# Optimization experiments

Measured on AMD Instinct MI355X. Metric: run time of the kernel, lower is better.

## Reference

```python
import jax, jax.numpy as jnp
import numpy as np

MAX_WORDS = 2048  # max word tokens per sequence (static num_segments)


def setup_inputs() -> dict:
    key = jax.random.key(0)
    k1, k2, k3, k4 = jax.random.split(key, 4)
    B, S, H, D = 8, 4096, 768, 1024
    embeddings = jax.random.normal(k1, (B, S, H), dtype=jnp.float32)
    proj_w = jax.random.normal(k2, (H, D), dtype=jnp.float32) * 0.02
    proj_b = jax.random.normal(k3, (D,), dtype=jnp.float32) * 0.02
    masks = jnp.ones((B, S), dtype=jnp.int32)
    word_ids = jnp.sort(jax.random.randint(k4, (B, S), 0, MAX_WORDS), axis=-1)
    return {"embeddings": embeddings, "proj_w": proj_w, "proj_b": proj_b,
            "masks": masks, "word_ids": word_ids}


def reference(embeddings, proj_w, proj_b, masks, word_ids):
    B, S, H = embeddings.shape
    W = MAX_WORDS
    # Flatten batch+word into one segment id space: seg in [0, B*W)
    seg = (word_ids + jnp.arange(B, dtype=word_ids.dtype)[:, None] * W).reshape(-1)
    flat_emb = embeddings.reshape(B * S, H)
    # segment-sum of embeddings over subwords of each word  -> (B, W, H)
    sum_emb = jax.ops.segment_sum(flat_emb, seg, num_segments=B * W).reshape(B, W, H)
    ones = jnp.ones((B * S,), dtype=jnp.float32)
    counts = jax.ops.segment_sum(ones, seg, num_segments=B * W).reshape(B, W)
    mcounts = jax.ops.segment_sum(masks.reshape(-1).astype(jnp.float32), seg,
                                  num_segments=B * W).reshape(B, W)
    # word is valid iff it has >=1 subword and ALL its subwords have mask==1
    valid = (counts > 0) & (counts == mcounts)
    mean_emb = sum_emb / jnp.maximum(counts, 1.0)[..., None]
    token_embeddings = jnp.where(valid[..., None], mean_emb, 0.0)  # (B, W, H)
    token_masks = valid.astype(jnp.int32)                          # (B, W)
    # projection: hidden 768 -> config.hidden_size 1024
    out = jnp.einsum('bwh,hd->bwd', token_embeddings, proj_w) + proj_b
    return out, token_masks
```

## Files before the change

### kernel.cpp

```cpp
#include <hip/hip_runtime.h>
#include <hip/hip_bf16.h>
#include <stdint.h>

#define Bn 8
#define Sn 4096
#define Hn 768
#define Dn 1024
#define Wn 2048

typedef __attribute__((ext_vector_type(8))) short short8;
typedef __attribute__((ext_vector_type(4))) short short4v;
typedef __attribute__((ext_vector_type(4))) float floatx4;

__device__ __forceinline__ void load_lds16(const void* g, void* l) {
  __builtin_amdgcn_global_load_lds(
      (const __attribute__((address_space(1))) void*)g,
      (__attribute__((address_space(3))) void*)l, 16, 0, 0);
}

__device__ __forceinline__ int lb4096(const int* __restrict__ a, int x, int lane) {
  const int p = a[lane << 6];
  const unsigned long long m1 = __ballot(p < x);
  const int n1 = __popcll(m1);
  const int base = (n1 > 0 ? n1 - 1 : 0) << 6;
  const int q = a[base + lane];
  const unsigned long long m2 = __ballot(q < x);
  return base + __popcll(m2);
}

__global__ __launch_bounds__(256) void k_front(const float* __restrict__ emb,
                                               const float* __restrict__ pw,
                                               const int* __restrict__ masks,
                                               const int* __restrict__ wid,
                                               __hip_bfloat16* __restrict__ wb,
                                               __hip_bfloat16* __restrict__ wa,
                                               float* __restrict__ out_masks) {
  const int bid = blockIdx.x;
  if (bid >= 4096) {
    __shared__ float tile[32][33];
    const int bt = bid - 4096;
    const int d0 = (bt % 32) * 32, h0 = (bt / 32) * 32;
    const int tx = threadIdx.x & 31, ty = threadIdx.x >> 5;
#pragma unroll
    for (int i = 0; i < 32; i += 8)
      tile[ty + i][tx] = pw[(size_t)(h0 + ty + i) * Dn + d0 + tx];
    __syncthreads();
#pragma unroll
    for (int i = 0; i < 32; i += 8)
      wb[(size_t)(d0 + ty + i) * Hn + h0 + tx] = (__hip_bfloat16)tile[tx][ty + i];
    return;
  }

  const int b = bid >> 9;
  const int wave = threadIdx.x >> 6, lane = threadIdx.x & 63;
  const int w = (bid & 511) * 4 + wave;

  const int* wbi = wid + (size_t)b * Sn;
  const int start = lb4096(wbi, w, lane);
  const int end = lb4096(wbi, w + 1, lane);
  const int count = end - start;

  const int* mb = masks + (size_t)b * Sn;
  bool allone = true;
  for (int s0 = start; s0 < end; s0 += 64) {
    const int idx = s0 + lane;
    allone = allone && ((idx < end) ? (mb[idx] == 1) : true);
  }
  const bool valid = (count > 0) && __all(allone);
  const float inv = valid ? 1.0f / (float)count : 0.0f;

  floatx4 sum[3] = {{0.f, 0.f, 0.f, 0.f}, {0.f, 0.f, 0.f, 0.f}, {0.f, 0.f, 0.f, 0.f}};
  const float* eb = emb + (size_t)b * Sn * Hn;
  int s = start;
  for (; s + 1 < end; s += 2) {
    const floatx4* r0 = (const floatx4*)(eb + (size_t)s * Hn);
    const floatx4* r1 = (const floatx4*)(eb + (size_t)(s + 1) * Hn);
#pragma unroll
    for (int j = 0; j < 3; ++j) sum[j] += r0[j * 64 + lane];
#pragma unroll
    for (int j = 0; j < 3; ++j) sum[j] += r1[j * 64 + lane];
  }
  if (s < end) {
    const floatx4* r0 = (const floatx4*)(eb + (size_t)s * Hn);
#pragma unroll
    for (int j = 0; j < 3; ++j) sum[j] += r0[j * 64 + lane];
  }

  const size_t rowbase = ((size_t)b * Wn + w) * Hn;
#pragma unroll
  for (int j = 0; j < 3; ++j) {
    short4v o;
#pragma unroll
    for (int c = 0; c < 4; ++c) {
      __hip_bfloat16 h = (__hip_bfloat16)(sum[j][c] * inv);
      o[c] = *reinterpret_cast<short*>(&h);
    }
    *(short4v*)&wa[rowbase + (size_t)(j * 64 + lane) * 4] = o;
  }
  if (lane == 0) out_masks[(size_t)b * Wn + w] = valid ? 1.0f : 0.0f;
}

__global__ __launch_bounds__(256) void k_gemm(const short* __restrict__ A,
                                              const short* __restrict__ Bt,
                                              const float* __restrict__ bias,
                                              float* __restrict__ out) {
  constexpr int K = Hn;
  constexpr int N = Dn;
  __shared__ __align__(16) short lsA[2][128 * 32];
  __shared__ __align__(16) short lsB[2][128 * 32];

  const int t = threadIdx.x;
  const int lane = t & 63, wave = t >> 6;
  const int wm = wave >> 1, wn = wave & 1;
  const int lane16 = lane & 15, quad = lane >> 4;

  const int linear = blockIdx.x;
  const int xcd = linear & 7;
  const int o = linear >> 3;
  const int m0 = (xcd * 16 + (o >> 3)) * 128;
  const int n0 = (o & 7) * 128;

  const int lrow = t >> 2;
  const int lcol = (t & 3) * 8;
  const short* gA0 = A + (size_t)(m0 + lrow) * K + lcol;
  const short* gB0 = Bt + (size_t)(n0 + lrow) * K + lcol;
  const int loff = lrow * 32 + lcol;

  float bv[4];
#pragma unroll
  for (int ni = 0; ni < 4; ++ni)
    bv[ni] = bias[n0 + wn * 64 + ni * 16 + lane16];

  floatx4 acc[4][4];
#pragma unroll
  for (int i = 0; i < 4; ++i)
#pragma unroll
    for (int j = 0; j < 4; ++j) acc[i][j] = (floatx4){0.f, 0.f, 0.f, 0.f};

  for (int k0 = 0; k0 < K; k0 += 64) {
    load_lds16(gA0 + k0,                    &lsA[0][loff]);
    load_lds16(gA0 + (size_t)64 * K + k0,   &lsA[0][loff + 64 * 32]);
    load_lds16(gA0 + k0 + 32,               &lsA[1][loff]);
    load_lds16(gA0 + (size_t)64 * K + k0 + 32, &lsA[1][loff + 64 * 32]);
    load_lds16(gB0 + k0,                    &lsB[0][loff]);
    load_lds16(gB0 + (size_t)64 * K + k0,   &lsB[0][loff + 64 * 32]);
    load_lds16(gB0 + k0 + 32,               &lsB[1][loff]);
    load_lds16(gB0 + (size_t)64 * K + k0 + 32, &lsB[1][loff + 64 * 32]);
    __syncthreads();

#pragma unroll
    for (int sp = 0; sp < 2; ++sp) {
      short8 af[4], bf[4];
#pragma unroll
      for (int mi = 0; mi < 4; ++mi)
        af[mi] = *(const short8*)&lsA[sp][(wm * 64 + mi * 16 + lane16) * 32 + quad * 8];
#pragma unroll
      for (int ni = 0; ni < 4; ++ni)
        bf[ni] = *(const short8*)&lsB[sp][(wn * 64 + ni * 16 + lane16) * 32 + quad * 8];

#pragma unroll
      for (int mi = 0; mi < 4; ++mi)
#pragma unroll
        for (int ni = 0; ni < 4; ++ni)
          acc[mi][ni] = __builtin_amdgcn_mfma_f32_16x16x32_bf16(af[mi], bf[ni], acc[mi][ni], 0, 0, 0);
    }
    __syncthreads();
  }

#pragma unroll
  for (int mi = 0; mi < 4; ++mi) {
#pragma unroll
    for (int ni = 0; ni < 4; ++ni) {
      const int n = n0 + wn * 64 + ni * 16 + lane16;
#pragma unroll
      for (int r = 0; r < 4; ++r) {
        const int m = m0 + wm * 64 + mi * 16 + quad * 4 + r;
        __builtin_nontemporal_store(acc[mi][ni][r] + bv[ni], &out[(size_t)m * N + n]);
      }
    }
  }
}

extern "C" void kernel_launch(void* const* d_in, const int* in_sizes, int n_in,
                              void* d_out, int out_size, void* d_ws, size_t ws_size,
                              hipStream_t stream) {
  const float* emb    = (const float*)d_in[0];
  const float* proj_w = (const float*)d_in[1];
  const float* proj_b = (const float*)d_in[2];
  const int*   masks  = (const int*)d_in[3];
  const int*   wid    = (const int*)d_in[4];

  float* out = (float*)d_out;
  float* out_masks = out + (size_t)Bn * Wn * Dn;

  __hip_bfloat16* wb = (__hip_bfloat16*)d_ws;
  __hip_bfloat16* wa = wb + (size_t)Dn * Hn;

  k_front<<<dim3(4096 + 768), 256, 0, stream>>>(emb, proj_w, masks, wid, wb, wa,
                                                out_masks);

  k_gemm<<<dim3(1024), 256, 0, stream>>>((const short*)wa, (const short*)wb,
                                         proj_b, out);
}
```

Baseline: 211.7 us.

## Rewrite GEMM with 256x256 tiles, swizzled LDS, and overlapped prefetch

Replaces the 128x128 GEMM tile with a 256x256 tile per 512-thread block, using 128 KB of dynamic LDS double-buffered across K steps of 64. LDS rows are XOR-swizzled to avoid bank conflicts. The next tile's global-to-LDS loads are issued between MFMA phases, and s_setprio raises priority during the MFMA sections. The aim is more data reuse and latency hiding, at the cost of only 256 blocks (one wave of work on 256 CUs) and higher register pressure.

Measured after the change: 205.0 us. 1.03x faster.

```diff
diff --git a/kernel.cpp b/kernel.cpp
--- a/kernel.cpp
+++ b/kernel.cpp
@@ -100,82 +100,122 @@
   if (lane == 0) out_masks[(size_t)b * Wn + w] = valid ? 1.0f : 0.0f;
 }
 
-__global__ __launch_bounds__(256) void k_gemm(const short* __restrict__ A,
-                                              const short* __restrict__ Bt,
-                                              const float* __restrict__ bias,
-                                              float* __restrict__ out) {
-  constexpr int K = Hn;
-  constexpr int N = Dn;
-  __shared__ __align__(16) short lsA[2][128 * 32];
-  __shared__ __align__(16) short lsB[2][128 * 32];
+constexpr int GK = Hn;
+constexpr int TS = 256 * 64;
+constexpr int kGemmLds = 2 * 2 * TS * (int)sizeof(short);
+static_assert(kGemmLds == 131072, "LDS budget");
+
+__global__ __launch_bounds__(512, 2) void k_gemm(const short* __restrict__ A,
+                                                 const short* __restrict__ Bt,
+                                                 const float* __restrict__ bias,
+                                                 float* __restrict__ out) {
+  extern __shared__ __align__(16) short ls[];
 
   const int t = threadIdx.x;
   const int lane = t & 63, wave = t >> 6;
-  const int wm = wave >> 1, wn = wave & 1;
+  const int wm = wave >> 2, wn = wave & 3;
   const int lane16 = lane & 15, quad = lane >> 4;
-
-  const int linear = blockIdx.x;
-  const int xcd = linear & 7;
-  const int o = linear >> 3;
-  const int m0 = (xcd * 16 + (o >> 3)) * 128;
-  const int n0 = (o & 7) * 128;
-
-  const int lrow = t >> 2;
-  const int lcol = (t & 3) * 8;
-  const short* gA0 = A + (size_t)(m0 + lrow) * K + lcol;
-  const short* gB0 = Bt + (size_t)(n0 + lrow) * K + lcol;
-  const int loff = lrow * 32 + lcol;
+  const int swz = lane16 & 7;
+
+  const int mt = blockIdx.x & 63, nt = blockIdx.x >> 6;
+  const int m0 = mt * 256, n0 = nt * 256;
+
+  const int rS = t >> 3;
+  const int csw = ((t & 7) ^ (rS & 7)) * 8;
+  const short* gAs = A + (size_t)(m0 + rS) * GK + csw;
+  const short* gBs = Bt + (size_t)(n0 + rS) * GK + csw;
+  const int dst0 = t * 8;
+
+  auto stage_a = [&](int buf, int kt) {
+    short* d = ls + buf * 2 * TS + dst0;
+    const short* g = gAs + kt * 64;
+#pragma unroll
+    for (int j = 0; j < 4; ++j) load_lds16(g + (size_t)(j * 64) * GK, d + j * 4096);
+  };
+  auto stage_b = [&](int buf, int kt) {
+    short* d = ls + buf * 2 * TS + TS + dst0;
+    const short* g = gBs + kt * 64;
+#pragma unroll
+    for (int j = 0; j < 4; ++j) load_lds16(g + (size_t)(j * 64) * GK, d + j * 4096);
+  };
+
+  auto ld_a = [&](short8(&af)[4][2], int qm, const short* bufA) {
+#pragma unroll
+    for (int mf = 0; mf < 4; ++mf)
+#pragma unroll
+      for (int ks = 0; ks < 2; ++ks)
+        af[mf][ks] = *(const short8*)&bufA[(wm * 128 + qm * 64 + mf * 16 + lane16) * 64 +
+                                           ((((ks << 2) | quad) ^ swz) << 3)];
+  };
+  auto ld_b = [&](short8(&bf)[2][2], int qn, const short* bufB) {
+#pragma unroll
+    for (int nf = 0; nf < 2; ++nf)
+#pragma unroll
+      for (int ks = 0; ks < 2; ++ks)
+        bf[nf][ks] = *(const short8*)&bufB[(wn * 64 + qn * 32 + nf * 16 + lane16) * 64 +
+                                           ((((ks << 2) | quad) ^ swz) << 3)];
+  };
+
+  floatx4 acc[8][4];
+#pragma unroll
+  for (int i = 0; i < 8; ++i)
+#pragma unroll
+    for (int j = 0; j < 4; ++j) acc[i][j] = (floatx4){0.f, 0.f, 0.f, 0.f};
+
+  auto mm = [&](short8(&af)[4][2], short8(&bf)[2][2], int qm, int qn) {
+    __builtin_amdgcn_s_setprio(1);
+#pragma unroll
+    for (int mf = 0; mf < 4; ++mf)
+#pragma unroll
+      for (int nf = 0; nf < 2; ++nf)
+#pragma unroll
+        for (int ks = 0; ks < 2; ++ks)
+          acc[qm * 4 + mf][qn * 2 + nf] = __builtin_amdgcn_mfma_f32_16x16x32_bf16(
+              af[mf][ks], bf[nf][ks], acc[qm * 4 + mf][qn * 2 + nf], 0, 0, 0);
+    __builtin_amdgcn_s_setprio(0);
+  };
+
+  stage_a(0, 0);
+  stage_b(0, 0);
+  __syncthreads();
+
+#pragma unroll 1
+  for (int kt = 0; kt < 12; ++kt) {
+    const short* bufA = ls + (kt & 1) * 2 * TS;
+    const short* bufB = bufA + TS;
+    const int nb = (kt + 1) & 1;
+    short8 af[4][2], b0[2][2], b1[2][2];
+
+    ld_a(af, 0, bufA);
+    ld_b(b0, 0, bufB);
+    if (kt < 11) stage_a(nb, kt + 1);
+    mm(af, b0, 0, 0);
+
+    ld_b(b1, 1, bufB);
+    if (kt < 11) stage_b(nb, kt + 1);
+    mm(af, b1, 0, 1);
+
+    ld_a(af, 1, bufA);
+    mm(af, b1, 1, 1);
+
+    mm(af, b0, 1, 0);
+
+    __syncthreads();
+  }
 
   float bv[4];
 #pragma unroll
-  for (int ni = 0; ni < 4; ++ni)
-    bv[ni] = bias[n0 + wn * 64 + ni * 16 + lane16];
-
-  floatx4 acc[4][4];
-#pragma unroll
-  for (int i = 0; i < 4; ++i)
-#pragma unroll
-    for (int j = 0; j < 4; ++j) acc[i][j] = (floatx4){0.f, 0.f, 0.f, 0.f};
-
-  for (int k0 = 0; k0 < K; k0 += 64) {
-    load_lds16(gA0 + k0,                    &lsA[0][loff]);
-    load_lds16(gA0 + (size_t)64 * K + k0,   &lsA[0][loff + 64 * 32]);
-    load_lds16(gA0 + k0 + 32,               &lsA[1][loff]);
-    load_lds16(gA0 + (size_t)64 * K + k0 + 32, &lsA[1][loff + 64 * 32]);
-    load_lds16(gB0 + k0,                    &lsB[0][loff]);
-    load_lds16(gB0 + (size_t)64 * K + k0,   &lsB[0][loff + 64 * 32]);
-    load_lds16(gB0 + k0 + 32,               &lsB[1][loff]);
-    load_lds16(gB0 + (size_t)64 * K + k0 + 32, &lsB[1][loff + 64 * 32]);
-    __syncthreads();
-
-#pragma unroll
-    for (int sp = 0; sp < 2; ++sp) {
-      short8 af[4], bf[4];
-#pragma unroll
-      for (int mi = 0; mi < 4; ++mi)
-        af[mi] = *(const short8*)&lsA[sp][(wm * 64 + mi * 16 + lane16) * 32 + quad * 8];
-#pragma unroll
-      for (int ni = 0; ni < 4; ++ni)
-        bf[ni] = *(const short8*)&lsB[sp][(wn * 64 + ni * 16 + lane16) * 32 + quad * 8];
-
-#pragma unroll
-      for (int mi = 0; mi < 4; ++mi)
-#pragma unroll
-        for (int ni = 0; ni < 4; ++ni)
-          acc[mi][ni] = __builtin_amdgcn_mfma_f32_16x16x32_bf16(af[mi], bf[ni], acc[mi][ni], 0, 0, 0);
-    }
-    __syncthreads();
-  }
-
-#pragma unroll
-  for (int mi = 0; mi < 4; ++mi) {
-#pragma unroll
-    for (int ni = 0; ni < 4; ++ni) {
-      const int n = n0 + wn * 64 + ni * 16 + lane16;
+  for (int nf = 0; nf < 4; ++nf) bv[nf] = bias[n0 + wn * 64 + nf * 16 + lane16];
+
+#pragma unroll
+  for (int mg = 0; mg < 8; ++mg) {
+#pragma unroll
+    for (int ng = 0; ng < 4; ++ng) {
+      const int n = n0 + wn * 64 + ng * 16 + lane16;
 #pragma unroll
       for (int r = 0; r < 4; ++r) {
-        const int m = m0 + wm * 64 + mi * 16 + quad * 4 + r;
-        __builtin_nontemporal_store(acc[mi][ni][r] + bv[ni], &out[(size_t)m * N + n]);
+        const int m = m0 + wm * 128 + mg * 16 + quad * 4 + r;
+        __builtin_nontemporal_store(acc[mg][ng][r] + bv[ng], &out[(size_t)m * Dn + n]);
       }
     }
   }
@@ -199,6 +239,8 @@
   k_front<<<dim3(4096 + 768), 256, 0, stream>>>(emb, proj_w, masks, wid, wb, wa,
                                                 out_masks);
 
-  k_gemm<<<dim3(1024), 256, 0, stream>>>((const short*)wa, (const short*)wb,
-                                         proj_b, out);
-}
+  (void)hipFuncSetAttribute((const void*)k_gemm,
+                            hipFuncAttributeMaxDynamicSharedMemorySize, kGemmLds);
+  k_gemm<<<dim3(256), 512, kGemmLds, stream>>>((const short*)wa, (const short*)wb,
+                                               proj_b, out);
+}
```
